# Kernel optimization log

Hardware: AMD Instinct MI355X
Metric: run time of the kernel (lower is better)

The kernel has to match this reference:

```python
import jax, jax.numpy as jnp
import numpy as np

EXP_SCALING = 10.0
N_HEAD = 16
KEY_SCALE_MAX = float(np.log(2 ** 16 - 1))


def setup_inputs() -> dict:
    key = jax.random.key(0)
    k1, k2, k3, k4 = jax.random.split(key, 4)
    B, T, C = 8, 2048, 1024
    nh = N_HEAD
    x = jax.random.normal(k1, (B, T, C), dtype=jnp.float32)
    Wk_weight = jax.random.normal(k2, (C, C), dtype=jnp.float32) * (1.0 / np.sqrt(C))
    # faithful to torch init: linspace(0.5, 5, nh)/10 and ones/10
    leaky_key_beta = (jnp.linspace(0.5, 5.0, nh, dtype=jnp.float32) / EXP_SCALING).reshape(1, nh, 1, 1)
    key_scale = jnp.ones((1, nh, 1, 1), dtype=jnp.float32) / EXP_SCALING
    return {"x": x, "Wk_weight": Wk_weight, "leaky_key_beta": leaky_key_beta,
            "key_scale": key_scale, "scale_pow": 1}


def reference(x, Wk_weight, leaky_key_beta, key_scale, scale_pow):
    B, T, C = x.shape
    nh = N_HEAD
    hs = C // nh
    # W_k projection + head split (the torch transpose/view dance is the standard split)
    k = (x @ Wk_weight.T).reshape(B, T, nh, hs).transpose(0, 2, 1, 3)  # (B, nh, T, hs)
    # LeakyAvg: coef[t, s] = exp(-(t - s) * beta_h) for s <= t, else 0
    beta = jnp.abs(leaky_key_beta).reshape(nh, 1, 1) * EXP_SCALING  # (nh, 1, 1)
    idx = jnp.arange(T)
    diff = idx[:, None] - idx[None, :]                # (T, T), >=0 below diag
    mask = diff >= 0
    diff_c = jnp.where(mask, diff, 0).astype(x.dtype)
    coef = jnp.exp(-diff_c * beta) * mask.astype(x.dtype)  # (nh, T, T) lower-triangular
    k = jnp.einsum('hts,bhsd->bhtd', coef, k)         # causal decay-weighted sum
    # L2 normalize along head dim
    k = k / (jnp.linalg.norm(k, axis=-1, keepdims=True) + 1e-10)
    # per-head learned scale, clamped in log-space
    scale = jnp.exp(jnp.minimum(scale_pow * EXP_SCALING * key_scale, KEY_SCALE_MAX))
    return k * scale
```

## Files before the change

kernel.cpp:

```cpp
#include <hip/hip_runtime.h>
#include <hip/hip_bf16.h>
#include <stdint.h>

#define B_SZ   8
#define T_SEQ  2048
#define C_DIM  1024
#define NH     16
#define HS     64
#define M_DIM  (B_SZ * T_SEQ)
#define EXP_SC 10.0f
#define KS_MAX 11.090339630053288f

typedef _Float16 f16;
typedef __attribute__((ext_vector_type(8))) _Float16 f16x8;
typedef __attribute__((ext_vector_type(4))) float f32x4;

__global__ void cast_f32_to_f16(const float* __restrict__ in,
                                f16* __restrict__ out, int n8) {
  int stride = gridDim.x * blockDim.x;
  for (int i = blockIdx.x * blockDim.x + threadIdx.x; i < n8; i += stride) {
    const float* p = in + (size_t)i * 8;
    float4 a = *(const float4*)p;
    float4 b = *(const float4*)(p + 4);
    f16x8 o;
    o[0] = (f16)a.x; o[1] = (f16)a.y; o[2] = (f16)a.z; o[3] = (f16)a.w;
    o[4] = (f16)b.x; o[5] = (f16)b.y; o[6] = (f16)b.z; o[7] = (f16)b.w;
    *(f16x8*)(out + (size_t)i * 8) = o;
  }
}

__device__ __forceinline__ void gl_lds16(const f16* g, const f16* l) {
  __builtin_amdgcn_global_load_lds(
      (const __attribute__((address_space(1))) void*)(uintptr_t)(const void*)g,
      (__attribute__((address_space(3))) void*)(uintptr_t)(const void*)l,
      16, 0, 0);
}

__global__ __launch_bounds__(256, 2)
void gemm_bt_f16(const f16* __restrict__ A,
                 const f16* __restrict__ Bt,
                 float* __restrict__ C) {
  __shared__ f16 As[128 * 32];
  __shared__ f16 Bs[128 * 32];

  const int tid = threadIdx.x;
  const int w = tid >> 6, l = tid & 63;
  const int bn = blockIdx.x & 7;
  const int bm = blockIdx.x >> 3;
  const int wm = w >> 1, wn = w & 1;

  const f32x4 zero = {0.f, 0.f, 0.f, 0.f};
  f32x4 acc[4][4];
#pragma unroll
  for (int i = 0; i < 4; ++i)
#pragma unroll
    for (int j = 0; j < 4; ++j) acc[i][j] = zero;

  const f16* Ag = A + (size_t)(bm * 128) * C_DIM;
  const f16* Bg = Bt + (size_t)(bn * 128) * C_DIM;

  const int fr = l & 15;
  const int fk = l >> 4;

  for (int k0 = 0; k0 < C_DIM; k0 += 32) {
    __syncthreads();
#pragma unroll
    for (int call = 0; call < 2; ++call) {
      int q = call * 256 + w * 64 + l;
      int r = q >> 2, c8 = (q & 3) << 3;
      const f16* ga = Ag + (size_t)r * C_DIM + k0 + c8;
      const f16* gb = Bg + (size_t)r * C_DIM + k0 + c8;
      const f16* la = As + (size_t)(call * 256 + w * 64) * 8;
      const f16* lb = Bs + (size_t)(call * 256 + w * 64) * 8;
      gl_lds16(ga, la);
      gl_lds16(gb, lb);
    }
    __syncthreads();

    f16x8 af[4], bfr[4];
#pragma unroll
    for (int i = 0; i < 4; ++i)
      af[i] = *(const f16x8*)(As + (wm * 64 + i * 16 + fr) * 32 + fk * 8);
#pragma unroll
    for (int j = 0; j < 4; ++j)
      bfr[j] = *(const f16x8*)(Bs + (wn * 64 + j * 16 + fr) * 32 + fk * 8);
#pragma unroll
    for (int i = 0; i < 4; ++i)
#pragma unroll
      for (int j = 0; j < 4; ++j)
        acc[i][j] = __builtin_amdgcn_mfma_f32_16x16x32_f16(af[i], bfr[j],
                                                           acc[i][j], 0, 0, 0);
  }

  const int orow0 = bm * 128 + wm * 64 + (l >> 4) * 4;
  const int ocol0 = bn * 128 + wn * 64 + (l & 15);
#pragma unroll
  for (int i = 0; i < 4; ++i)
#pragma unroll
    for (int j = 0; j < 4; ++j)
#pragma unroll
      for (int r = 0; r < 4; ++r)
        C[(size_t)(orow0 + i * 16 + r) * C_DIM + ocol0 + j * 16] = acc[i][j][r];
}

__global__ __launch_bounds__(256)
void scan_norm(const float* __restrict__ kbuf,
               const float* __restrict__ beta_p,
               const float* __restrict__ ks_p,
               const int* __restrict__ sp_p,
               float* __restrict__ out) {
  const int l = threadIdx.x & 63;
  const int gw = blockIdx.x * 4 + (threadIdx.x >> 6);
  const int c = gw & 31;
  const int h = (gw >> 5) & 15;
  const int b = gw >> 9;

  const float beta = fabsf(beta_p[h]) * EXP_SC;
  const float a = expf(-beta);
  const float sp = (float)sp_p[0];
  const float scale = expf(fminf(sp * EXP_SC * ks_p[h], KS_MAX));

  const float* kp = kbuf + (size_t)b * T_SEQ * C_DIM + h * HS + l;
  float* op = out + ((size_t)(b * NH + h) * T_SEQ) * HS + l;

  const int t0 = c * 64;
  float y = 0.f;
  int s = (t0 >= 64) ? (t0 - 64) : 0;
#pragma unroll 8
  for (; s < t0; ++s)
    y = fmaf(a, y, kp[(size_t)s * C_DIM]);

#pragma unroll 4
  for (int t = t0; t < t0 + 64; ++t) {
    y = fmaf(a, y, kp[(size_t)t * C_DIM]);
    float sq = y * y;
#pragma unroll
    for (int m = 1; m < 64; m <<= 1)
      sq += __shfl_xor(sq, m, 64);
    float nrm = sqrtf(sq) + 1e-10f;
    op[(size_t)t * HS] = y * (scale / nrm);
  }
}

extern "C" void kernel_launch(void* const* d_in, const int* in_sizes, int n_in,
                              void* d_out, int out_size, void* d_ws, size_t ws_size,
                              hipStream_t stream) {
  const float* x      = (const float*)d_in[0];
  const float* Wk     = (const float*)d_in[1];
  const float* beta   = (const float*)d_in[2];
  const float* kscale = (const float*)d_in[3];
  const int*   spow   = (const int*)d_in[4];
  float* out = (float*)d_out;

  f16* x_h = (f16*)d_ws;
  f16* W_h = x_h + (size_t)M_DIM * C_DIM;
  float* kbuf = (float*)(W_h + (size_t)C_DIM * C_DIM);

  cast_f32_to_f16<<<2048, 256, 0, stream>>>(x, x_h, (M_DIM * C_DIM) / 8);
  cast_f32_to_f16<<<512, 256, 0, stream>>>(Wk, W_h, (C_DIM * C_DIM) / 8);
  gemm_bt_f16<<<dim3((M_DIM / 128) * (C_DIM / 128)), 256, 0, stream>>>(x_h, W_h, kbuf);
  scan_norm<<<1024, 256, 0, stream>>>(kbuf, beta, kscale, spow, out);
}
```

Baseline: 212.8 us.

## Double-buffer GEMM LDS tiles, remap blocks across XCDs, merge cast kernels

The GEMM now stages K-tiles into two LDS buffers, issuing the next tile's global-to-LDS loads before computing on the current one. This halves the barriers per step and overlaps memory latency with MFMA work. Block IDs are remapped so that consecutive workgroups, which are spread round-robin over XCDs, share A rows within an XCD for better L2 reuse. The two f32-to-f16 cast kernels are merged into one launch. LDS use doubles to 32KB per block, which may limit occupancy, and the single barrier per step relies on the hardware waiting for outstanding global_load_lds operations at __syncthreads.

```diff
diff --git a/kernel.cpp b/kernel.cpp
--- a/kernel.cpp
+++ b/kernel.cpp
@@ -15,17 +15,27 @@
 typedef __attribute__((ext_vector_type(8))) _Float16 f16x8;
 typedef __attribute__((ext_vector_type(4))) float f32x4;
 
-__global__ void cast_f32_to_f16(const float* __restrict__ in,
-                                f16* __restrict__ out, int n8) {
+__global__ void cast_two(const float* __restrict__ xin, f16* __restrict__ xout, int n8x,
+                         const float* __restrict__ win, f16* __restrict__ wout, int n8w) {
   int stride = gridDim.x * blockDim.x;
-  for (int i = blockIdx.x * blockDim.x + threadIdx.x; i < n8; i += stride) {
-    const float* p = in + (size_t)i * 8;
+  int t0 = blockIdx.x * blockDim.x + threadIdx.x;
+  for (int i = t0; i < n8x; i += stride) {
+    const float* p = xin + (size_t)i * 8;
     float4 a = *(const float4*)p;
     float4 b = *(const float4*)(p + 4);
     f16x8 o;
     o[0] = (f16)a.x; o[1] = (f16)a.y; o[2] = (f16)a.z; o[3] = (f16)a.w;
     o[4] = (f16)b.x; o[5] = (f16)b.y; o[6] = (f16)b.z; o[7] = (f16)b.w;
-    *(f16x8*)(out + (size_t)i * 8) = o;
+    *(f16x8*)(xout + (size_t)i * 8) = o;
+  }
+  for (int i = t0; i < n8w; i += stride) {
+    const float* p = win + (size_t)i * 8;
+    float4 a = *(const float4*)p;
+    float4 b = *(const float4*)(p + 4);
+    f16x8 o;
+    o[0] = (f16)a.x; o[1] = (f16)a.y; o[2] = (f16)a.z; o[3] = (f16)a.w;
+    o[4] = (f16)b.x; o[5] = (f16)b.y; o[6] = (f16)b.z; o[7] = (f16)b.w;
+    *(f16x8*)(wout + (size_t)i * 8) = o;
   }
 }
 
@@ -40,13 +50,17 @@
 void gemm_bt_f16(const f16* __restrict__ A,
                  const f16* __restrict__ Bt,
                  float* __restrict__ C) {
-  __shared__ f16 As[128 * 32];
-  __shared__ f16 Bs[128 * 32];
+  __shared__ f16 As[2][128 * 32];
+  __shared__ f16 Bs[2][128 * 32];
 
   const int tid = threadIdx.x;
   const int w = tid >> 6, l = tid & 63;
-  const int bn = blockIdx.x & 7;
-  const int bm = blockIdx.x >> 3;
+
+  const int q = blockIdx.x;
+  const int wgid = (q & 7) * 128 + (q >> 3);
+  const int bm = wgid >> 3;
+  const int bn = wgid & 7;
+
   const int wm = w >> 1, wn = w & 1;
 
   const f32x4 zero = {0.f, 0.f, 0.f, 0.f};
@@ -59,38 +73,46 @@
   const f16* Ag = A + (size_t)(bm * 128) * C_DIM;
   const f16* Bg = Bt + (size_t)(bn * 128) * C_DIM;
 
+  const int r0  = (w * 64 + l) >> 2;
+  const int c8  = ((w * 64 + l) & 3) << 3;
+  const int lo0 = (w * 64 + l) * 8;
+
   const int fr = l & 15;
   const int fk = l >> 4;
 
-  for (int k0 = 0; k0 < C_DIM; k0 += 32) {
-    __syncthreads();
-#pragma unroll
-    for (int call = 0; call < 2; ++call) {
-      int q = call * 256 + w * 64 + l;
-      int r = q >> 2, c8 = (q & 3) << 3;
-      const f16* ga = Ag + (size_t)r * C_DIM + k0 + c8;
-      const f16* gb = Bg + (size_t)r * C_DIM + k0 + c8;
-      const f16* la = As + (size_t)(call * 256 + w * 64) * 8;
-      const f16* lb = Bs + (size_t)(call * 256 + w * 64) * 8;
-      gl_lds16(ga, la);
-      gl_lds16(gb, lb);
-    }
-    __syncthreads();
+#define STAGE(buf, k0)                                                   \
+  do {                                                                   \
+    gl_lds16(Ag + (size_t)r0 * C_DIM + (k0) + c8,        As[buf] + lo0); \
+    gl_lds16(Bg + (size_t)r0 * C_DIM + (k0) + c8,        Bs[buf] + lo0); \
+    gl_lds16(Ag + (size_t)(r0 + 64) * C_DIM + (k0) + c8, As[buf] + lo0 + 2048); \
+    gl_lds16(Bg + (size_t)(r0 + 64) * C_DIM + (k0) + c8, Bs[buf] + lo0 + 2048); \
+  } while (0)
+
+  STAGE(0, 0);
+  __syncthreads();
+
+  int cur = 0;
+  for (int step = 0; step < 32; ++step) {
+    if (step + 1 < 32) STAGE(cur ^ 1, (step + 1) * 32);
 
     f16x8 af[4], bfr[4];
 #pragma unroll
     for (int i = 0; i < 4; ++i)
-      af[i] = *(const f16x8*)(As + (wm * 64 + i * 16 + fr) * 32 + fk * 8);
+      af[i] = *(const f16x8*)(As[cur] + (wm * 64 + i * 16 + fr) * 32 + fk * 8);
 #pragma unroll
     for (int j = 0; j < 4; ++j)
-      bfr[j] = *(const f16x8*)(Bs + (wn * 64 + j * 16 + fr) * 32 + fk * 8);
+      bfr[j] = *(const f16x8*)(Bs[cur] + (wn * 64 + j * 16 + fr) * 32 + fk * 8);
 #pragma unroll
     for (int i = 0; i < 4; ++i)
 #pragma unroll
       for (int j = 0; j < 4; ++j)
         acc[i][j] = __builtin_amdgcn_mfma_f32_16x16x32_f16(af[i], bfr[j],
                                                            acc[i][j], 0, 0, 0);
+
+    __syncthreads();
+    cur ^= 1;
   }
+#undef STAGE
 
   const int orow0 = bm * 128 + wm * 64 + (l >> 4) * 4;
   const int ocol0 = bn * 128 + wn * 64 + (l & 15);
@@ -156,8 +178,8 @@
   f16* W_h = x_h + (size_t)M_DIM * C_DIM;
   float* kbuf = (float*)(W_h + (size_t)C_DIM * C_DIM);
 
-  cast_f32_to_f16<<<2048, 256, 0, stream>>>(x, x_h, (M_DIM * C_DIM) / 8);
-  cast_f32_to_f16<<<512, 256, 0, stream>>>(Wk, W_h, (C_DIM * C_DIM) / 8);
+  cast_two<<<2048, 256, 0, stream>>>(x, x_h, (M_DIM * C_DIM) / 8,
+                                     Wk, W_h, (C_DIM * C_DIM) / 8);
   gemm_bt_f16<<<dim3((M_DIM / 128) * (C_DIM / 128)), 256, 0, stream>>>(x_h, W_h, kbuf);
   scan_norm<<<1024, 256, 0, stream>>>(kbuf, beta, kscale, spow, out);
 }
```

Measured after the change: 205.2 us. 3.6% less time.
